# Kernel optimization log

Measured on AMD Instinct MI355X. Metric: run time of the kernel, lower is better.

Reference implementation:

```python
import jax, jax.numpy as jnp
import numpy as np

N = 50000      # nodes
E = 800000     # edges
D_IN = 256     # state_dim
H = 128        # HIDDEN_LAYER
A = 32         # action_dim
EPS = 1e-5
NEG_SLOPE = 0.2


def setup_inputs() -> dict:
    key = jax.random.key(0)
    ks = jax.random.split(key, 16)
    s = lambda k, shape, std=0.1: jax.random.normal(k, shape, jnp.float32) * std
    return {
        "x": jax.random.normal(ks[0], (N, D_IN), jnp.float32),
        "edge_index": jax.random.randint(ks[1], (2, E), 0, N, jnp.int64),
        # GAT params
        "W": s(ks[2], (D_IN, H)),
        "a_src": s(ks[3], (H,)),
        "a_dst": s(ks[4], (H,)),
        "b_gat": jnp.zeros((H,), jnp.float32),
        # bn0
        "g0": jnp.ones((H,), jnp.float32),
        "beta0": jnp.zeros((H,), jnp.float32),
        # fc1, fc2
        "W1": s(ks[5], (H, H)),
        "b1": jnp.zeros((H,), jnp.float32),
        "W2": s(ks[6], (H, H)),
        "b2": jnp.zeros((H,), jnp.float32),
        # bn2
        "g2": jnp.ones((H,), jnp.float32),
        "beta2": jnp.zeros((H,), jnp.float32),
        # fc3
        "W3": s(ks[7], (H, A)),
        "b3": jnp.zeros((A,), jnp.float32),
    }


def _batchnorm(h, gamma, beta):
    # training-mode BN: biased batch stats over node dim
    mu = jnp.mean(h, axis=0)
    var = jnp.var(h, axis=0)
    return (h - mu) * jax.lax.rsqrt(var + EPS) * gamma + beta


def _gat(x, edge_index, W, a_src, a_dst, b_gat):
    src, dst = edge_index[0], edge_index[1]
    h = x @ W                                  # [N, H]
    e_src = h @ a_src                          # [N]
    e_dst = h @ a_dst                          # [N]
    e = jax.nn.leaky_relu(e_src[src] + e_dst[dst], NEG_SLOPE)  # [E]
    # neighbor softmax over edges grouped by destination node
    m = jax.ops.segment_max(e, dst, num_segments=N)            # [N]
    w = jnp.exp(e - m[dst])                                    # [E]
    denom = jax.ops.segment_sum(w, dst, num_segments=N)        # [N]
    alpha = w / jnp.maximum(denom, 1e-16)[dst]                 # [E]
    out = jax.ops.segment_sum(alpha[:, None] * h[src], dst, num_segments=N)
    return out + b_gat


def reference(x, edge_index, W, a_src, a_dst, b_gat, g0, beta0,
              W1, b1, W2, b2, g2, beta2, W3, b3):
    h0 = jax.nn.relu(_gat(x, edge_index, W, a_src, a_dst, b_gat))
    h0n = _batchnorm(h0, g0, beta0)
    h1 = jax.nn.relu(h0n @ W1 + b1)
    h2 = jax.nn.relu(h1 @ W2 + b2)
    h2n = _batchnorm(h2, g2, beta2)
    action = h2n @ W3 + b3
    return jax.nn.softmax(action, axis=1)
```

## Files before the change

kernel.cpp:

```cpp
#include <hip/hip_runtime.h>
#include <math.h>

#define N_NODES 50000
#define N_EDGES 800000
#define D_INPUT 256
#define HDIM 128
#define A_DIM 32
#define NEG_SLOPE 0.2f
#define BN_EPS 1e-5f
#define CAP 64
#define NB 391
#define BIN_SHIFT 7
#define BCAP 2432
#define GC_STRIDE 16
#define EPB 4096

typedef short short8 __attribute__((ext_vector_type(8)));
typedef unsigned short ushort8v __attribute__((ext_vector_type(8)));
typedef unsigned short ushort4v __attribute__((ext_vector_type(4)));
typedef float float4v __attribute__((ext_vector_type(4)));

__device__ __forceinline__ unsigned short f2bf(float f) {
  unsigned u = __float_as_uint(f);
  u += 0x7FFFu + ((u >> 16) & 1u);
  return (unsigned short)(u >> 16);
}
__device__ __forceinline__ float bf2f(unsigned short b) {
  return __uint_as_float(((unsigned)b) << 16);
}

__device__ __forceinline__ float waveReduceMax(float v) {
#pragma unroll
  for (int o = 32; o >= 1; o >>= 1) v = fmaxf(v, __shfl_xor(v, o, 64));
  return v;
}
__device__ __forceinline__ float waveReduceSum(float v) {
#pragma unroll
  for (int o = 32; o >= 1; o >>= 1) v += __shfl_xor(v, o, 64);
  return v;
}

__global__ __launch_bounds__(256) void k_prep(
    const float* __restrict__ W, const float* __restrict__ W1,
    const float* __restrict__ W2, unsigned short* __restrict__ Wt0,
    unsigned short* __restrict__ Wt1, unsigned short* __restrict__ Wt2)
{
  int i = blockIdx.x * 256 + threadIdx.x;
  if (i < HDIM * D_INPUT) {
    int n = i >> 8, k = i & 255;
    Wt0[i] = f2bf(W[(size_t)k * HDIM + n]);
  }
  if (i < HDIM * HDIM) {
    int n = i >> 7, k = i & 127;
    Wt1[i] = f2bf(W1[(size_t)k * HDIM + n]);
    Wt2[i] = f2bf(W2[(size_t)k * HDIM + n]);
  }
}

__global__ __launch_bounds__(256) void k_gemm_xw_mfma(
    const float* __restrict__ x, const unsigned short* __restrict__ Wt0,
    const float* __restrict__ a_src, const float* __restrict__ a_dst,
    unsigned short* __restrict__ hbf, float* __restrict__ esrc, float* __restrict__ edst)
{
  __shared__ short As[64][72];
  __shared__ short Bs[128][72];
  __shared__ float esred[64][2], edred[64][2];

  const int t = threadIdx.x;
  const int lane = t & 63;
  const int wv = t >> 6;
  const int rh = wv >> 1;
  const int ch = wv & 1;
  const int quad = (lane >> 4) & 3;
  const int l15 = lane & 15;
  const int row0 = blockIdx.x * 64;

  float4v acc[2][4];
#pragma unroll
  for (int i = 0; i < 2; ++i)
#pragma unroll
    for (int j = 0; j < 4; ++j) acc[i][j] = (float4v){0.f, 0.f, 0.f, 0.f};

  for (int ks = 0; ks < D_INPUT / 64; ++ks) {
    const int kk0 = ks * 64;
#pragma unroll
    for (int it = 0; it < 4; ++it) {
      int idx = it * 256 + t;
      int r = idx >> 4, c4 = idx & 15;
      int rr = row0 + r; if (rr >= N_NODES) rr = N_NODES - 1;
      float4 v = *(const float4*)(x + (size_t)rr * D_INPUT + kk0 + c4 * 4);
      ushort4v b; b.x = f2bf(v.x); b.y = f2bf(v.y); b.z = f2bf(v.z); b.w = f2bf(v.w);
      *(ushort4v*)(&As[r][c4 * 4]) = b;
    }
#pragma unroll
    for (int it = 0; it < 4; ++it) {
      int idx = it * 256 + t;
      int n = idx >> 3, c8 = idx & 7;
      *(ushort8v*)(&Bs[n][c8 * 8]) = *(const ushort8v*)(Wt0 + (size_t)n * D_INPUT + kk0 + c8 * 8);
    }
    __syncthreads();
#pragma unroll
    for (int kc = 0; kc < 2; ++kc) {
      short8 af[2], bfr[4];
#pragma unroll
      for (int rt = 0; rt < 2; ++rt)
        af[rt] = *(const short8*)(&As[rh * 32 + rt * 16 + l15][kc * 32 + quad * 8]);
#pragma unroll
      for (int nt = 0; nt < 4; ++nt)
        bfr[nt] = *(const short8*)(&Bs[ch * 64 + nt * 16 + l15][kc * 32 + quad * 8]);
#pragma unroll
      for (int rt = 0; rt < 2; ++rt)
#pragma unroll
        for (int nt = 0; nt < 4; ++nt)
          acc[rt][nt] = __builtin_amdgcn_mfma_f32_16x16x32_bf16(af[rt], bfr[nt], acc[rt][nt], 0, 0, 0);
    }
    __syncthreads();
  }

  float asv[4], adv[4];
#pragma unroll
  for (int nt = 0; nt < 4; ++nt) {
    int col = ch * 64 + nt * 16 + l15;
    asv[nt] = a_src[col]; adv[nt] = a_dst[col];
  }
#pragma unroll
  for (int rt = 0; rt < 2; ++rt) {
#pragma unroll
    for (int reg = 0; reg < 4; ++reg) {
      int rloc = rh * 32 + rt * 16 + quad * 4 + reg;
      int row = row0 + rloc;
      bool valid = (row < N_NODES);
      float ps = 0.f, pd = 0.f;
#pragma unroll
      for (int nt = 0; nt < 4; ++nt) {
        float v = acc[rt][nt][reg];
        ps += v * asv[nt]; pd += v * adv[nt];
        if (valid) hbf[(size_t)row * HDIM + ch * 64 + nt * 16 + l15] = f2bf(v);
      }
#pragma unroll
      for (int o = 8; o >= 1; o >>= 1) {
        ps += __shfl_xor(ps, o, 64);
        pd += __shfl_xor(pd, o, 64);
      }
      if (l15 == 0) { esred[rloc][ch] = ps; edred[rloc][ch] = pd; }
    }
  }
  __syncthreads();
  if (t < 64) {
    int row = row0 + t;
    if (row < N_NODES) {
      esrc[row] = esred[t][0] + esred[t][1];
      edst[row] = edred[t][0] + edred[t][1];
    }
  }
}

__global__ __launch_bounds__(256) void k_bin(
    const int* __restrict__ srcI, const int* __restrict__ dstI,
    int* __restrict__ gcur, int* __restrict__ bbuf)
{
  __shared__ int hist[NB];
  __shared__ int base[NB];
  const int t = threadIdx.x;
  const int e0 = blockIdx.x * EPB;
  const int e1 = min(e0 + EPB, N_EDGES);
  for (int i = t; i < NB; i += 256) hist[i] = 0;
  __syncthreads();
  for (int e = e0 + t; e < e1; e += 256)
    atomicAdd(&hist[dstI[e] >> BIN_SHIFT], 1);
  __syncthreads();
  for (int i = t; i < NB; i += 256) {
    base[i] = atomicAdd(&gcur[i * GC_STRIDE], hist[i]);
    hist[i] = 0;
  }
  __syncthreads();
  for (int e = e0 + t; e < e1; e += 256) {
    int d = dstI[e];
    int bin = d >> BIN_SHIFT;
    int r = atomicAdd(&hist[bin], 1) + base[bin];
    if (r < BCAP) bbuf[(size_t)bin * BCAP + r] = srcI[e] | ((d & 127) << 16);
  }
}

__global__ __launch_bounds__(256) void k_sc2(
    const int* __restrict__ gcur, const int* __restrict__ bbuf,
    const float* __restrict__ esrc, const float* __restrict__ edst,
    int* __restrict__ deg, int2* __restrict__ sedge)
{
  __shared__ int2 bk[128][CAP];
  __shared__ int lcur[128];
  __shared__ float ledst[128];
  const int t = threadIdx.x;
  const int bin = blockIdx.x;
  const int d0 = bin << BIN_SHIFT;
  if (t < 128) {
    lcur[t] = 0;
    int d = d0 + t;
    ledst[t] = (d < N_NODES) ? edst[d] : 0.f;
  }
  __syncthreads();
  const int cnt = min(gcur[bin * GC_STRIDE], BCAP);
  const int* seg = bbuf + (size_t)bin * BCAP;
  for (int i = t; i < cnt; i += 256) {
    int v = seg[i];
    int s = v & 0xFFFF;
    int dl = (v >> 16) & 127;
    float ev = esrc[s] + ledst[dl];
    ev = (ev > 0.f) ? ev : NEG_SLOPE * ev;
    int r = atomicAdd(&lcur[dl], 1);
    if (r < CAP) {
      int2 e2; e2.x = s; e2.y = __float_as_int(ev);
      bk[dl][r] = e2;
    }
  }
  __syncthreads();
  for (int idx = t; idx < 128 * CAP; idx += 256) {
    int dl = idx >> 6, sl = idx & 63;
    if (sl < lcur[dl])
      sedge[(size_t)(d0 + dl) * CAP + sl] = bk[dl][sl];
  }
  if (t < 128) {
    int d = d0 + t;
    if (d < N_NODES) deg[d] = min(lcur[t], CAP);
  }
}

__global__ __launch_bounds__(256) void k_agg(
    const int* __restrict__ degA, const int2* __restrict__ sedge,
    const unsigned short* __restrict__ hbf,
    const float* __restrict__ b_gat, unsigned short* __restrict__ h0)
{
  const int t = threadIdx.x;
  const int lane = t & 63;
  const int node = blockIdx.x * 4 + (t >> 6);
  const int deg = min(degA[node], CAP);

  int2 ev; ev.x = 0; ev.y = 0;
  float val = -INFINITY;
  if (lane < deg) {
    ev = sedge[(size_t)node * CAP + lane];
    val = __int_as_float(ev.y);
  }
  const float m = waveReduceMax(val);
  const float ex = (lane < deg) ? __expf(val - m) : 0.f;
  const float s = waveReduceSum(ex);
  const float al = ex * (1.0f / fmaxf(s, 1e-16f));
  const int sr = ev.x;

  float ax = 0.f, ay = 0.f;
  int j = 0;
  for (; j + 4 <= deg; j += 4) {
    float a0 = __shfl(al, j, 64),   a1 = __shfl(al, j+1, 64);
    float a2 = __shfl(al, j+2, 64), a3 = __shfl(al, j+3, 64);
    int s0 = __shfl(sr, j, 64),   s1 = __shfl(sr, j+1, 64);
    int s2 = __shfl(sr, j+2, 64), s3 = __shfl(sr, j+3, 64);
    unsigned v0 = *(const unsigned*)(hbf + (size_t)s0 * HDIM + lane * 2);
    unsigned v1 = *(const unsigned*)(hbf + (size_t)s1 * HDIM + lane * 2);
    unsigned v2 = *(const unsigned*)(hbf + (size_t)s2 * HDIM + lane * 2);
    unsigned v3 = *(const unsigned*)(hbf + (size_t)s3 * HDIM + lane * 2);
    ax += a0 * bf2f((unsigned short)(v0 & 0xFFFFu))
        + a1 * bf2f((unsigned short)(v1 & 0xFFFFu))
        + a2 * bf2f((unsigned short)(v2 & 0xFFFFu))
        + a3 * bf2f((unsigned short)(v3 & 0xFFFFu));
    ay += a0 * bf2f((unsigned short)(v0 >> 16))
        + a1 * bf2f((unsigned short)(v1 >> 16))
        + a2 * bf2f((unsigned short)(v2 >> 16))
        + a3 * bf2f((unsigned short)(v3 >> 16));
  }
  for (; j < deg; ++j) {
    float a = __shfl(al, j, 64);
    int sj = __shfl(sr, j, 64);
    unsigned v = *(const unsigned*)(hbf + (size_t)sj * HDIM + lane * 2);
    ax += a * bf2f((unsigned short)(v & 0xFFFFu));
    ay += a * bf2f((unsigned short)(v >> 16));
  }
  float vx = fmaxf(ax + b_gat[lane * 2], 0.f);
  float vy = fmaxf(ay + b_gat[lane * 2 + 1], 0.f);
  *(unsigned*)(h0 + (size_t)node * HDIM + lane * 2) =
      (unsigned)f2bf(vx) | ((unsigned)f2bf(vy) << 16);
}

#define BN_ROWS 256
__global__ __launch_bounds__(256) void k_bnstats(
    const unsigned short* __restrict__ src, float* __restrict__ gsum, float* __restrict__ gsq)
{
  __shared__ float red[16][128];
  const int t = threadIdx.x;
  const int cg = t & 15;
  const int rl = t >> 4;
  const int row0 = blockIdx.x * BN_ROWS;
  float s[8], q[8];
#pragma unroll
  for (int j = 0; j < 8; ++j) { s[j] = 0.f; q[j] = 0.f; }
  for (int i = 0; i < BN_ROWS / 16; ++i) {
    int row = row0 + rl + i * 16;
    if (row < N_NODES) {
      ushort8v v = *(const ushort8v*)(src + (size_t)row * HDIM + cg * 8);
#pragma unroll
      for (int j = 0; j < 8; ++j) {
        float f = bf2f(v[j]);
        s[j] += f; q[j] += f * f;
      }
    }
  }
#pragma unroll
  for (int j = 0; j < 8; ++j) red[rl][cg * 8 + j] = s[j];
  __syncthreads();
  if (t < 128) {
    float S = 0.f;
#pragma unroll
    for (int r = 0; r < 16; ++r) S += red[r][t];
    atomicAdd(&gsum[t], S);
  }
  __syncthreads();
#pragma unroll
  for (int j = 0; j < 8; ++j) red[rl][cg * 8 + j] = q[j];
  __syncthreads();
  if (t < 128) {
    float Q = 0.f;
#pragma unroll
    for (int r = 0; r < 16; ++r) Q += red[r][t];
    atomicAdd(&gsq[t], Q);
  }
}

__global__ __launch_bounds__(256) void k_fc12(
    const unsigned short* __restrict__ in,
    const float* __restrict__ gsumIn, const float* __restrict__ gsqIn,
    const float* __restrict__ gamma, const float* __restrict__ beta,
    const unsigned short* __restrict__ Wt1, const float* __restrict__ b1,
    const unsigned short* __restrict__ Wt2, const float* __restrict__ b2,
    unsigned short* __restrict__ outp,
    float* __restrict__ gsum, float* __restrict__ gsq)
{
  __shared__ short As[64 * 72];
  __shared__ short Bsh[128 * 72];
  __shared__ short H1[64 * 136];
  __shared__ float statS[128][2], statQ[128][2];
  __shared__ float sc[HDIM], shf[HDIM];

  const int t = threadIdx.x;
  const int lane = t & 63;
  const int wv = t >> 6;
  const int rh = wv >> 1;
  const int ch = wv & 1;
  const int quad = (lane >> 4) & 3;
  const int l15 = lane & 15;
  const int row0 = blockIdx.x * 64;

  if (t < HDIM) {
    float mean = gsumIn[t] / (float)N_NODES;
    float var = gsqIn[t] / (float)N_NODES - mean * mean;
    float s = gamma[t] * rsqrtf(var + BN_EPS);
    sc[t] = s; shf[t] = beta[t] - mean * s;
  }
  __syncthreads();

  float4v acc[2][4];
#pragma unroll
  for (int i = 0; i < 2; ++i)
#pragma unroll
    for (int j = 0; j < 4; ++j) acc[i][j] = (float4v){0.f, 0.f, 0.f, 0.f};

  for (int ks = 0; ks < 2; ++ks) {
    const int kk0 = ks * 64;
#pragma unroll
    for (int it = 0; it < 2; ++it) {
      int idx = it * 256 + t;
      int r = idx >> 3, c8 = idx & 7;
      int rr = row0 + r; if (rr >= N_NODES) rr = N_NODES - 1;
      ushort8v v = *(const ushort8v*)(in + (size_t)rr * HDIM + kk0 + c8 * 8);
#pragma unroll
      for (int j = 0; j < 8; ++j) {
        int k = kk0 + c8 * 8 + j;
        v[j] = f2bf(bf2f(v[j]) * sc[k] + shf[k]);
      }
      *(ushort8v*)(&As[r * 72 + c8 * 8]) = v;
    }
#pragma unroll
    for (int it = 0; it < 4; ++it) {
      int idx = it * 256 + t;
      int n = idx >> 3, c8 = idx & 7;
      *(ushort8v*)(&Bsh[n * 72 + c8 * 8]) = *(const ushort8v*)(Wt1 + (size_t)n * HDIM + kk0 + c8 * 8);
    }
    __syncthreads();
#pragma unroll
    for (int kc = 0; kc < 2; ++kc) {
      short8 af[2], bfr[4];
#pragma unroll
      for (int rt = 0; rt < 2; ++rt)
        af[rt] = *(const short8*)(&As[(rh * 32 + rt * 16 + l15) * 72 + kc * 32 + quad * 8]);
#pragma unroll
      for (int nt = 0; nt < 4; ++nt)
        bfr[nt] = *(const short8*)(&Bsh[(ch * 64 + nt * 16 + l15) * 72 + kc * 32 + quad * 8]);
#pragma unroll
      for (int rt = 0; rt < 2; ++rt)
#pragma unroll
        for (int nt = 0; nt < 4; ++nt)
          acc[rt][nt] = __builtin_amdgcn_mfma_f32_16x16x32_bf16(af[rt], bfr[nt], acc[rt][nt], 0, 0, 0);
    }
    __syncthreads();
  }

  {
    float bv[4];
#pragma unroll
    for (int nt = 0; nt < 4; ++nt) bv[nt] = b1[ch * 64 + nt * 16 + l15];
#pragma unroll
    for (int rt = 0; rt < 2; ++rt) {
#pragma unroll
      for (int reg = 0; reg < 4; ++reg) {
        int rloc = rh * 32 + rt * 16 + quad * 4 + reg;
#pragma unroll
        for (int nt = 0; nt < 4; ++nt) {
          float o = fmaxf(acc[rt][nt][reg] + bv[nt], 0.f);
          H1[rloc * 136 + ch * 64 + nt * 16 + l15] = f2bf(o);
        }
      }
    }
  }
  __syncthreads();

#pragma unroll
  for (int i = 0; i < 2; ++i)
#pragma unroll
    for (int j = 0; j < 4; ++j) acc[i][j] = (float4v){0.f, 0.f, 0.f, 0.f};

  for (int ks = 0; ks < 2; ++ks) {
    const int kk0 = ks * 64;
#pragma unroll
    for (int it = 0; it < 4; ++it) {
      int idx = it * 256 + t;
      int n = idx >> 3, c8 = idx & 7;
      *(ushort8v*)(&Bsh[n * 72 + c8 * 8]) = *(const ushort8v*)(Wt2 + (size_t)n * HDIM + kk0 + c8 * 8);
    }
    __syncthreads();
#pragma unroll
    for (int kc = 0; kc < 2; ++kc) {
      short8 af[2], bfr[4];
#pragma unroll
      for (int rt = 0; rt < 2; ++rt)
        af[rt] = *(const short8*)(&H1[(rh * 32 + rt * 16 + l15) * 136 + kk0 + kc * 32 + quad * 8]);
#pragma unroll
      for (int nt = 0; nt < 4; ++nt)
        bfr[nt] = *(const short8*)(&Bsh[(ch * 64 + nt * 16 + l15) * 72 + kc * 32 + quad * 8]);
#pragma unroll
      for (int rt = 0; rt < 2; ++rt)
#pragma unroll
        for (int nt = 0; nt < 4; ++nt)
          acc[rt][nt] = __builtin_amdgcn_mfma_f32_16x16x32_bf16(af[rt], bfr[nt], acc[rt][nt], 0, 0, 0);
    }
    __syncthreads();
  }

  float bv[4];
#pragma unroll
  for (int nt = 0; nt < 4; ++nt) bv[nt] = b2[ch * 64 + nt * 16 + l15];

  float pS[4] = {0.f, 0.f, 0.f, 0.f}, pQ[4] = {0.f, 0.f, 0.f, 0.f};
#pragma unroll
  for (int rt = 0; rt < 2; ++rt) {
#pragma unroll
    for (int reg = 0; reg < 4; ++reg) {
      int row = row0 + rh * 32 + rt * 16 + quad * 4 + reg;
      bool valid = (row < N_NODES);
#pragma unroll
      for (int nt = 0; nt < 4; ++nt) {
        float o = fmaxf(acc[rt][nt][reg] + bv[nt], 0.f);
        if (valid) {
          outp[(size_t)row * HDIM + ch * 64 + nt * 16 + l15] = f2bf(o);
          pS[nt] += o; pQ[nt] += o * o;
        }
      }
    }
  }
#pragma unroll
  for (int nt = 0; nt < 4; ++nt) {
    float s = pS[nt], q = pQ[nt];
    s += __shfl_xor(s, 16, 64); s += __shfl_xor(s, 32, 64);
    q += __shfl_xor(q, 16, 64); q += __shfl_xor(q, 32, 64);
    if (lane < 16) {
      statS[ch * 64 + nt * 16 + lane][rh] = s;
      statQ[ch * 64 + nt * 16 + lane][rh] = q;
    }
  }
  __syncthreads();
  if (t < 128) {
    atomicAdd(&gsum[t], statS[t][0] + statS[t][1]);
    atomicAdd(&gsq[t],  statQ[t][0] + statQ[t][1]);
  }
}

__global__ __launch_bounds__(256) void k_fc3(
    const unsigned short* __restrict__ h2,
    const float* __restrict__ gsumIn, const float* __restrict__ gsqIn,
    const float* __restrict__ gamma, const float* __restrict__ beta,
    const float* __restrict__ W3, const float* __restrict__ b3,
    float* __restrict__ out)
{
  __shared__ float w3s[HDIM * A_DIM];
  __shared__ float s2[HDIM], sh2[HDIM];
  __shared__ unsigned short hr[8][HDIM];
  const int t = threadIdx.x;
  for (int l = t; l < HDIM * A_DIM; l += 256) w3s[l] = W3[l];
  if (t < HDIM) {
    float mean = gsumIn[t] / (float)N_NODES;
    float var = gsqIn[t] / (float)N_NODES - mean * mean;
    float s = gamma[t] * rsqrtf(var + BN_EPS);
    s2[t] = s; sh2[t] = beta[t] - mean * s;
  }
  const int rbase = blockIdx.x * 8;
  if (t < 128) {
    int rr = t >> 4, cg = t & 15;
    int row = rbase + rr;
    if (row < N_NODES)
      *(ushort8v*)(&hr[rr][cg * 8]) =
          *(const ushort8v*)(h2 + (size_t)row * HDIM + cg * 8);
  }
  __syncthreads();

  const int j = t & 31;
  const int rloc = t >> 5;
  const int row = rbase + rloc;
  if (row >= N_NODES) return;

  float dotv = 0.f;
#pragma unroll 4
  for (int k = 0; k < HDIM; ++k) {
    float hv = bf2f(hr[rloc][k]) * s2[k] + sh2[k];
    dotv += hv * w3s[k * A_DIM + j];
  }
  float logit = dotv + b3[j];
  float mx = logit;
#pragma unroll
  for (int o = 16; o >= 1; o >>= 1) mx = fmaxf(mx, __shfl_xor(mx, o, 32));
  float ex = __expf(logit - mx);
  float sm = ex;
#pragma unroll
  for (int o = 16; o >= 1; o >>= 1) sm += __shfl_xor(sm, o, 32);
  out[(size_t)row * A_DIM + j] = ex / sm;
}

extern "C" void kernel_launch(void* const* d_in, const int* in_sizes, int n_in,
                              void* d_out, int out_size, void* d_ws, size_t ws_size,
                              hipStream_t stream) {
  const float* x     = (const float*)d_in[0];
  const int*   ei    = (const int*)d_in[1];
  const float* W     = (const float*)d_in[2];
  const float* a_src = (const float*)d_in[3];
  const float* a_dst = (const float*)d_in[4];
  const float* b_gat = (const float*)d_in[5];
  const float* g0    = (const float*)d_in[6];
  const float* beta0 = (const float*)d_in[7];
  const float* W1    = (const float*)d_in[8];
  const float* b1    = (const float*)d_in[9];
  const float* W2    = (const float*)d_in[10];
  const float* b2    = (const float*)d_in[11];
  const float* g2    = (const float*)d_in[12];
  const float* beta2 = (const float*)d_in[13];
  const float* W3    = (const float*)d_in[14];
  const float* b3    = (const float*)d_in[15];
  float* out = (float*)d_out;
  const int* srcI = ei;
  const int* dstI = ei + N_EDGES;

  char* p = (char*)d_ws;
  auto alloc = [&](size_t bytes) -> char* {
    char* q = p; p += (bytes + 255) & ~(size_t)255; return q;
  };
  unsigned short* h   = (unsigned short*)alloc(sizeof(short) * (size_t)N_NODES * HDIM);
  unsigned short* h0  = (unsigned short*)alloc(sizeof(short) * (size_t)N_NODES * HDIM);
  unsigned short* h2  = h;
  unsigned short* Wt0 = (unsigned short*)alloc(sizeof(short) * HDIM * D_INPUT);
  unsigned short* Wt1 = (unsigned short*)alloc(sizeof(short) * HDIM * HDIM);
  unsigned short* Wt2 = (unsigned short*)alloc(sizeof(short) * HDIM * HDIM);
  int2*  sedge  = (int2*)alloc(sizeof(int2) * (size_t)N_NODES * CAP);
  int*   bbuf   = (int*)alloc(sizeof(int) * (size_t)NB * BCAP);
  float* esrc   = (float*)alloc(sizeof(float) * N_NODES);
  float* edst   = (float*)alloc(sizeof(float) * N_NODES);
  int*   deg    = (int*)alloc(sizeof(int) * N_NODES);
  char*  zbase  = alloc(sizeof(int) * NB * GC_STRIDE + 256 + sizeof(float) * 4 * 128);
  int*   gcur   = (int*)zbase;
  float* stats  = (float*)(zbase + ((sizeof(int) * NB * GC_STRIDE + 255) & ~(size_t)255));
  float* gsum0 = stats;        float* gsq0  = stats + 128;
  float* gsum2 = stats + 256;  float* gsq2  = stats + 384;
  size_t zsize = (size_t)((char*)(stats + 512) - zbase);

  hipMemsetAsync(zbase, 0, zsize, stream);

  const int gT = (N_NODES + 63) / 64;
  const int gB = (N_EDGES + EPB - 1) / EPB;

  k_prep<<<(HDIM * D_INPUT + 255) / 256, 256, 0, stream>>>(W, W1, W2, Wt0, Wt1, Wt2);
  k_gemm_xw_mfma<<<gT, 256, 0, stream>>>(x, Wt0, a_src, a_dst, h, esrc, edst);
  k_bin<<<gB, 256, 0, stream>>>(srcI, dstI, gcur, bbuf);
  k_sc2<<<NB, 256, 0, stream>>>(gcur, bbuf, esrc, edst, deg, sedge);
  k_agg<<<N_NODES / 4, 256, 0, stream>>>(deg, sedge, h, b_gat, h0);
  k_bnstats<<<(N_NODES + BN_ROWS - 1) / BN_ROWS, 256, 0, stream>>>(h0, gsum0, gsq0);
  k_fc12<<<gT, 256, 0, stream>>>(h0, gsum0, gsq0, g0, beta0, Wt1, b1, Wt2, b2, h2,
                                 gsum2, gsq2);
  k_fc3<<<(N_NODES + 7) / 8, 256, 0, stream>>>(h2, gsum2, gsq2, g2, beta2, W3, b3, out);
}
```

Before: 281.3 us.

## Merge weight prep into binning launch and register-tile the final FC/softmax

```diff
diff --git a/kernel.cpp b/kernel.cpp
--- a/kernel.cpp
+++ b/kernel.cpp
@@ -14,6 +14,7 @@
 #define BCAP 2432
 #define GC_STRIDE 16
 #define EPB 4096
+#define FC3_TR 64
 
 typedef short short8 __attribute__((ext_vector_type(8)));
 typedef unsigned short ushort8v __attribute__((ext_vector_type(8)));
@@ -38,23 +39,6 @@
 #pragma unroll
   for (int o = 32; o >= 1; o >>= 1) v += __shfl_xor(v, o, 64);
   return v;
-}
-
-__global__ __launch_bounds__(256) void k_prep(
-    const float* __restrict__ W, const float* __restrict__ W1,
-    const float* __restrict__ W2, unsigned short* __restrict__ Wt0,
-    unsigned short* __restrict__ Wt1, unsigned short* __restrict__ Wt2)
-{
-  int i = blockIdx.x * 256 + threadIdx.x;
-  if (i < HDIM * D_INPUT) {
-    int n = i >> 8, k = i & 255;
-    Wt0[i] = f2bf(W[(size_t)k * HDIM + n]);
-  }
-  if (i < HDIM * HDIM) {
-    int n = i >> 7, k = i & 127;
-    Wt1[i] = f2bf(W1[(size_t)k * HDIM + n]);
-    Wt2[i] = f2bf(W2[(size_t)k * HDIM + n]);
-  }
 }
 
 __global__ __launch_bounds__(256) void k_gemm_xw_mfma(
@@ -155,10 +139,27 @@
   }
 }
 
-__global__ __launch_bounds__(256) void k_bin(
+__global__ __launch_bounds__(256) void k_binprep(
     const int* __restrict__ srcI, const int* __restrict__ dstI,
-    int* __restrict__ gcur, int* __restrict__ bbuf)
+    int* __restrict__ gcur, int* __restrict__ bbuf,
+    const float* __restrict__ W, const float* __restrict__ W1,
+    const float* __restrict__ W2, unsigned short* __restrict__ Wt0,
+    unsigned short* __restrict__ Wt1, unsigned short* __restrict__ Wt2)
 {
+  const int gB = (N_EDGES + EPB - 1) / EPB;
+  if (blockIdx.x >= gB) {
+    int i = (blockIdx.x - gB) * 256 + threadIdx.x;
+    if (i < HDIM * D_INPUT) {
+      int n = i >> 8, k = i & 255;
+      Wt0[i] = f2bf(W[(size_t)k * HDIM + n]);
+    }
+    if (i < HDIM * HDIM) {
+      int n = i >> 7, k = i & 127;
+      Wt1[i] = f2bf(W1[(size_t)k * HDIM + n]);
+      Wt2[i] = f2bf(W2[(size_t)k * HDIM + n]);
+    }
+    return;
+  }
   __shared__ int hist[NB];
   __shared__ int base[NB];
   const int t = threadIdx.x;
@@ -491,54 +492,98 @@
   }
 }
 
-__global__ __launch_bounds__(256) void k_fc3(
+__global__ __launch_bounds__(128) void k_fc3(
     const unsigned short* __restrict__ h2,
     const float* __restrict__ gsumIn, const float* __restrict__ gsqIn,
     const float* __restrict__ gamma, const float* __restrict__ beta,
     const float* __restrict__ W3, const float* __restrict__ b3,
     float* __restrict__ out)
 {
-  __shared__ float w3s[HDIM * A_DIM];
-  __shared__ float s2[HDIM], sh2[HDIM];
-  __shared__ unsigned short hr[8][HDIM];
+  __shared__ float w3p[HDIM][A_DIM];
+  __shared__ float hs[HDIM][FC3_TR + 2];
+  __shared__ float s2s[HDIM], sh2s[HDIM];
+  __shared__ float bred[4][A_DIM];
+  __shared__ float b3p[A_DIM];
   const int t = threadIdx.x;
-  for (int l = t; l < HDIM * A_DIM; l += 256) w3s[l] = W3[l];
-  if (t < HDIM) {
+
+  {
     float mean = gsumIn[t] / (float)N_NODES;
     float var = gsqIn[t] / (float)N_NODES - mean * mean;
     float s = gamma[t] * rsqrtf(var + BN_EPS);
-    s2[t] = s; sh2[t] = beta[t] - mean * s;
-  }
-  const int rbase = blockIdx.x * 8;
-  if (t < 128) {
-    int rr = t >> 4, cg = t & 15;
-    int row = rbase + rr;
-    if (row < N_NODES)
-      *(ushort8v*)(&hr[rr][cg * 8]) =
-          *(const ushort8v*)(h2 + (size_t)row * HDIM + cg * 8);
-  }
-  __syncthreads();
-
-  const int j = t & 31;
-  const int rloc = t >> 5;
-  const int row = rbase + rloc;
-  if (row >= N_NODES) return;
-
-  float dotv = 0.f;
-#pragma unroll 4
-  for (int k = 0; k < HDIM; ++k) {
-    float hv = bf2f(hr[rloc][k]) * s2[k] + sh2[k];
-    dotv += hv * w3s[k * A_DIM + j];
-  }
-  float logit = dotv + b3[j];
-  float mx = logit;
-#pragma unroll
-  for (int o = 16; o >= 1; o >>= 1) mx = fmaxf(mx, __shfl_xor(mx, o, 32));
-  float ex = __expf(logit - mx);
-  float sm = ex;
-#pragma unroll
-  for (int o = 16; o >= 1; o >>= 1) sm += __shfl_xor(sm, o, 32);
-  out[(size_t)row * A_DIM + j] = ex / sm;
+    s2s[t] = s; sh2s[t] = beta[t] - mean * s;
+  }
+  __syncthreads();
+
+  for (int i = t; i < HDIM * A_DIM; i += 128) {
+    int k = i >> 5;
+    w3p[k][i & 31] = s2s[k] * W3[i];
+  }
+  {
+    int j = t & 31, seg = t >> 5;
+    float p = 0.f;
+    for (int kk = 0; kk < 32; ++kk) {
+      int k = seg * 32 + kk;
+      p += sh2s[k] * W3[k * A_DIM + j];
+    }
+    bred[seg][j] = p;
+  }
+  const int row0 = blockIdx.x * FC3_TR;
+  for (int i = t; i < FC3_TR * (HDIM / 8); i += 128) {
+    int r = i & 63, cg = i >> 6;
+    int row = row0 + r;
+    ushort8v v;
+    if (row < N_NODES) v = *(const ushort8v*)(h2 + (size_t)row * HDIM + cg * 8);
+    else { for (int jj = 0; jj < 8; ++jj) v[jj] = 0; }
+#pragma unroll
+    for (int jj = 0; jj < 8; ++jj) hs[cg * 8 + jj][r] = bf2f(v[jj]);
+  }
+  __syncthreads();
+  if (t < 32) b3p[t] = b3[t] + bred[0][t] + bred[1][t] + bred[2][t] + bred[3][t];
+  __syncthreads();
+
+  const int r0 = (t >> 3) * 4;
+  const int j0 = (t & 7) * 4;
+  float4 acc[4];
+#pragma unroll
+  for (int r = 0; r < 4; ++r) acc[r] = (float4){0.f, 0.f, 0.f, 0.f};
+
+  for (int k = 0; k < HDIM; k += 4) {
+    float4 w0 = *(const float4*)&w3p[k + 0][j0];
+    float4 w1 = *(const float4*)&w3p[k + 1][j0];
+    float4 w2 = *(const float4*)&w3p[k + 2][j0];
+    float4 w3v = *(const float4*)&w3p[k + 3][j0];
+#pragma unroll
+    for (int r = 0; r < 4; ++r) {
+      int rr = r0 + r;
+      float h0 = hs[k + 0][rr], h1 = hs[k + 1][rr];
+      float h2v = hs[k + 2][rr], h3 = hs[k + 3][rr];
+      acc[r].x += h0 * w0.x + h1 * w1.x + h2v * w2.x + h3 * w3v.x;
+      acc[r].y += h0 * w0.y + h1 * w1.y + h2v * w2.y + h3 * w3v.y;
+      acc[r].z += h0 * w0.z + h1 * w1.z + h2v * w2.z + h3 * w3v.z;
+      acc[r].w += h0 * w0.w + h1 * w1.w + h2v * w2.w + h3 * w3v.w;
+    }
+  }
+
+  float4 b4 = *(const float4*)&b3p[j0];
+#pragma unroll
+  for (int r = 0; r < 4; ++r) {
+    float l0 = acc[r].x + b4.x, l1 = acc[r].y + b4.y;
+    float l2 = acc[r].z + b4.z, l3 = acc[r].w + b4.w;
+    float mx = fmaxf(fmaxf(l0, l1), fmaxf(l2, l3));
+#pragma unroll
+    for (int o = 1; o <= 4; o <<= 1) mx = fmaxf(mx, __shfl_xor(mx, o, 64));
+    float e0 = __expf(l0 - mx), e1 = __expf(l1 - mx);
+    float e2 = __expf(l2 - mx), e3 = __expf(l3 - mx);
+    float sm = e0 + e1 + e2 + e3;
+#pragma unroll
+    for (int o = 1; o <= 4; o <<= 1) sm += __shfl_xor(sm, o, 64);
+    float inv = 1.0f / sm;
+    int row = row0 + r0 + r;
+    if (row < N_NODES) {
+      float4 o4; o4.x = e0 * inv; o4.y = e1 * inv; o4.z = e2 * inv; o4.w = e3 * inv;
+      *(float4*)(out + (size_t)row * A_DIM + j0) = o4;
+    }
+  }
 }
 
 extern "C" void kernel_launch(void* const* d_in, const int* in_sizes, int n_in,
@@ -590,14 +635,16 @@
 
   const int gT = (N_NODES + 63) / 64;
   const int gB = (N_EDGES + EPB - 1) / EPB;
-
-  k_prep<<<(HDIM * D_INPUT + 255) / 256, 256, 0, stream>>>(W, W1, W2, Wt0, Wt1, Wt2);
+  const int gP = (HDIM * D_INPUT + 255) / 256;
+
+  k_binprep<<<gB + gP, 256, 0, stream>>>(srcI, dstI, gcur, bbuf,
+                                         W, W1, W2, Wt0, Wt1, Wt2);
   k_gemm_xw_mfma<<<gT, 256, 0, stream>>>(x, Wt0, a_src, a_dst, h, esrc, edst);
-  k_bin<<<gB, 256, 0, stream>>>(srcI, dstI, gcur, bbuf);
   k_sc2<<<NB, 256, 0, stream>>>(gcur, bbuf, esrc, edst, deg, sedge);
   k_agg<<<N_NODES / 4, 256, 0, stream>>>(deg, sedge, h, b_gat, h0);
   k_bnstats<<<(N_NODES + BN_ROWS - 1) / BN_ROWS, 256, 0, stream>>>(h0, gsum0, gsq0);
   k_fc12<<<gT, 256, 0, stream>>>(h0, gsum0, gsq0, g0, beta0, Wt1, b1, Wt2, b2, h2,
                                  gsum2, gsq2);
-  k_fc3<<<(N_NODES + 7) / 8, 256, 0, stream>>>(h2, gsum2, gsq2, g2, beta2, W3, b3, out);
-}
+  k_fc3<<<(N_NODES + FC3_TR - 1) / FC3_TR, 128, 0, stream>>>(
+      h2, gsum2, gsq2, g2, beta2, W3, b3, out);
+}
```

New measurement: 265.9 us. -5.5%, faster.
